# Kernel tuning notes

Measured on AMD Instinct MI355X. Metric: run time of the kernel, lower is better.

The kernel has to match this reference:

```python
import jax, jax.numpy as jnp
import numpy as np

B, S, D, H = 2, 2048, 1024, 16
DK = D // H  # 64
SCALE = DK ** (-0.5)  # NOTE: module divides by this, i.e. multiplies scores by sqrt(DK)


def setup_inputs() -> dict:
    key = jax.random.key(0)
    ks = jax.random.split(key, 9)
    std = D ** (-0.5)
    return {
        "x": jax.random.normal(ks[0], (B, S, D), dtype=jnp.float32),
        "attention_mask": jnp.ones((B, S), dtype=jnp.int32),
        "Wq": jax.random.normal(ks[1], (D, D), dtype=jnp.float32) * std,
        "bq": jnp.zeros((D,), dtype=jnp.float32),
        "Wk": jax.random.normal(ks[2], (D, D), dtype=jnp.float32) * std,
        "bk": jnp.zeros((D,), dtype=jnp.float32),
        "Wv": jax.random.normal(ks[3], (D, D), dtype=jnp.float32) * std,
        "bv": jnp.zeros((D,), dtype=jnp.float32),
        "Wo": jax.random.normal(ks[4], (D, D), dtype=jnp.float32) * std,
        "bo": jnp.zeros((D,), dtype=jnp.float32),
    }


def _split_heads(t):
    # [B, S, D] -> [B, H, S, DK]
    return t.reshape(B, S, H, DK).transpose(0, 2, 1, 3)


def reference(x, attention_mask, Wq, bq, Wk, bk, Wv, bv, Wo, bo):
    q = _split_heads(x @ Wq.T + bq)
    k = _split_heads(x @ Wk.T + bk)
    v = _split_heads(x @ Wv.T + bv)

    # faithful to source: sim = (q @ k^T) / scale with scale = dk**-0.5
    sim = jnp.einsum("bhqd,bhkd->bhqk", q, k) / SCALE

    # key-padding mask: positions where attention_mask == 0 are masked out
    neg = jnp.finfo(sim.dtype).min
    keep = attention_mask.astype(bool)[:, None, None, :]  # [B,1,1,S]
    sim = jnp.where(keep, sim, neg)

    attn = jax.nn.softmax(sim, axis=-1)  # dropout is identity at inference
    out = jnp.einsum("bhqk,bhkd->bhqd", attn, v)
    out = out.transpose(0, 2, 1, 3).reshape(B, S, D)  # merge heads
    return out @ Wo.T + bo
```

## Files before the change

### kernel.cpp

```cpp
#include <hip/hip_runtime.h>
#include <hip/hip_bf16.h>
#include <math.h>

#define BB 2
#define SS 2048
#define DD 1024
#define HH 16
#define DKK 64
#define BH (BB * HH)

typedef __bf16 bf16_t;
typedef _Float16 f16_t;
typedef __attribute__((ext_vector_type(8))) _Float16 f16x8;
typedef __attribute__((ext_vector_type(4))) _Float16 f16x4;
typedef __attribute__((ext_vector_type(4))) float f32x4;
typedef __attribute__((ext_vector_type(4))) int i32x4;
typedef __attribute__((ext_vector_type(2))) int i32x2;

#define GLD_LDS(gp, lp) __builtin_amdgcn_global_load_lds( \
    (const __attribute__((address_space(1))) void*)(gp),  \
    (__attribute__((address_space(3))) void*)(lp), 16, 0, 0)

static __device__ __forceinline__ int pkrtz(float a, float b) {
    auto h = __builtin_amdgcn_cvt_pkrtz(a, b);
    return __builtin_bit_cast(int, h);
}

__global__ void prep_all(const float* __restrict__ x, const int* __restrict__ mask,
                         const float* __restrict__ Wq, const float* __restrict__ Wk,
                         const float* __restrict__ Wv, const float* __restrict__ Wo,
                         f16_t* __restrict__ xf,
                         f16_t* __restrict__ wqkh, f16_t* __restrict__ wqkl,
                         f16_t* __restrict__ wvf, f16_t* __restrict__ wof,
                         int* __restrict__ flags) {
    const int NXi = BB * SS * DD;
    const int NWi = DD * DD;
    const int total = NXi + 4 * NWi;
    int i = blockIdx.x * blockDim.x + threadIdx.x;
    const int stride = gridDim.x * blockDim.x;
    for (; i < total; i += stride) {
        if (i < NXi) {
            xf[i] = (f16_t)x[i];
        } else if (i < NXi + 2 * NWi) {
            const int j = i - NXi;
            const float v = (j < NWi) ? Wq[j] : Wk[j - NWi];
            const f16_t h = (f16_t)v;
            wqkh[j] = h;
            wqkl[j] = (f16_t)(v - (float)h);
        } else {
            const int j = i - NXi - 2 * NWi;
            if (j < NWi) wvf[j] = (f16_t)Wv[j];
            else         wof[j - NWi] = (f16_t)Wo[j - NWi];
        }
    }
    if (blockIdx.x == 0 && threadIdx.x < BB * (SS / 128)) {
        const int f = threadIdx.x;
        const int b = f / (SS / 128), t = f % (SS / 128);
        const int* p = mask + b * SS + t * 128;
        int all = 1;
        for (int j = 0; j < 128; ++j) all &= (p[j] != 0);
        flags[f] = all;
    }
}

__global__ __launch_bounds__(256) void gemm_qkv(const f16_t* __restrict__ Af,
                                                const f16_t* __restrict__ Wqkh,
                                                const f16_t* __restrict__ Wqkl,
                                                const f16_t* __restrict__ Wvf,
                                                const float* __restrict__ bq,
                                                const float* __restrict__ bk,
                                                const float* __restrict__ bv,
                                                f16_t* __restrict__ q_o,
                                                f16_t* __restrict__ k_o,
                                                f16_t* __restrict__ vt_o,
                                                int K) {
    __shared__ __align__(16) f16_t sA[8192];
    __shared__ __align__(16) f16_t sB0[8192];
    __shared__ __align__(16) f16_t sB1[8192];

    const int tid  = threadIdx.x;
    const int wv   = tid >> 6;
    const int lane = tid & 63;
    const int quad = lane >> 4;
    const int l15  = lane & 15;
    const int wr   = wv >> 1;
    const int wc   = wv & 1;
    const int row0 = blockIdx.y * 128;
    const int col0 = blockIdx.x * 128;
    const bool isV = (col0 >= 2048);

    const f16_t* B0 = isV ? (Wvf + (long)(col0 - 2048) * K) : (Wqkh + (long)col0 * K);
    const f16_t* B1 = isV ? nullptr : (Wqkl + (long)col0 * K);

    f32x4 acc[4][4] = {};

    const int srow8 = lane >> 3;
    const int gsw   = ((lane & 7) ^ srow8) * 8;
    const long aoff = (long)(row0 + wv * 8 + srow8) * K + gsw;
    const long boff = (long)(wv * 8 + srow8) * K + gsw;
    const int lsw   = l15 & 7;

    if (isV) {
#pragma unroll 1
        for (int kb = 0; kb < K; kb += 64) {
#pragma unroll
            for (int p = 0; p < 4; ++p) {
                const long go = (long)p * 32 * K + kb;
                const int lo = p * 2048 + wv * 512;
                GLD_LDS(Af + aoff + go, sA + lo);
                GLD_LDS(B0 + boff + go, sB0 + lo);
            }
            __syncthreads();
#pragma unroll
            for (int kk = 0; kk < 2; ++kk) {
                f16x8 af[4];
#pragma unroll
                for (int mt = 0; mt < 4; ++mt)
                    af[mt] = *(const f16x8*)&sA[(wr * 64 + mt * 16 + l15) * 64 + (((kk * 4 + quad) ^ lsw) << 3)];
#pragma unroll
                for (int nt = 0; nt < 4; ++nt) {
                    f16x8 b0 = *(const f16x8*)&sB0[(wc * 64 + nt * 16 + l15) * 64 + (((kk * 4 + quad) ^ lsw) << 3)];
#pragma unroll
                    for (int mt = 0; mt < 4; ++mt)
                        acc[mt][nt] = __builtin_amdgcn_mfma_f32_16x16x32_f16(af[mt], b0, acc[mt][nt], 0, 0, 0);
                }
            }
            __syncthreads();
        }
    } else {
#pragma unroll 1
        for (int kb = 0; kb < K; kb += 64) {
#pragma unroll
            for (int p = 0; p < 4; ++p) {
                const long go = (long)p * 32 * K + kb;
                const int lo = p * 2048 + wv * 512;
                GLD_LDS(Af + aoff + go, sA + lo);
                GLD_LDS(B0 + boff + go, sB0 + lo);
                GLD_LDS(B1 + boff + go, sB1 + lo);
            }
            __syncthreads();
#pragma unroll
            for (int kk = 0; kk < 2; ++kk) {
                f16x8 af[4];
#pragma unroll
                for (int mt = 0; mt < 4; ++mt)
                    af[mt] = *(const f16x8*)&sA[(wr * 64 + mt * 16 + l15) * 64 + (((kk * 4 + quad) ^ lsw) << 3)];
#pragma unroll
                for (int nt = 0; nt < 4; ++nt) {
                    f16x8 b0 = *(const f16x8*)&sB0[(wc * 64 + nt * 16 + l15) * 64 + (((kk * 4 + quad) ^ lsw) << 3)];
                    f16x8 b1 = *(const f16x8*)&sB1[(wc * 64 + nt * 16 + l15) * 64 + (((kk * 4 + quad) ^ lsw) << 3)];
#pragma unroll
                    for (int mt = 0; mt < 4; ++mt) {
                        acc[mt][nt] = __builtin_amdgcn_mfma_f32_16x16x32_f16(af[mt], b0, acc[mt][nt], 0, 0, 0);
                        acc[mt][nt] = __builtin_amdgcn_mfma_f32_16x16x32_f16(af[mt], b1, acc[mt][nt], 0, 0, 0);
                    }
                }
            }
            __syncthreads();
        }
    }

    if (isV) {
#pragma unroll
        for (int nt = 0; nt < 4; ++nt) {
            const int colv = (col0 - 2048) + wc * 64 + nt * 16 + l15;
            const float bvv = bv[colv];
            const int hq = colv >> 6, dk = colv & 63;
#pragma unroll
            for (int mt = 0; mt < 4; ++mt) {
                const int grow0 = row0 + wr * 64 + mt * 16 + quad * 4;
                const int bq2 = grow0 >> 11;
                const int s0  = grow0 & (SS - 1);
                f16x4 pk;
#pragma unroll
                for (int r = 0; r < 4; ++r) pk[r] = (f16_t)(acc[mt][nt][r] + bvv);
                *(f16x4*)(vt_o + ((long)(bq2 * HH + hq) * DKK + dk) * SS + s0) = pk;
            }
        }
    } else {
        const bool isK = (col0 >= 1024);
        const float* bias = isK ? bk : bq;
        f16_t* op = isK ? k_o : q_o;
#pragma unroll
        for (int nt = 0; nt < 4; ++nt) {
            const int gcol = (col0 & 1023) + wc * 64 + nt * 16 + l15;
            const float bvv = bias[gcol];
            const int hq = gcol >> 6, dk = gcol & 63;
#pragma unroll
            for (int mt = 0; mt < 4; ++mt) {
                const int grow0 = row0 + wr * 64 + mt * 16 + quad * 4;
#pragma unroll
                for (int r = 0; r < 4; ++r) {
                    int grow = grow0 + r;
                    float vvv = acc[mt][nt][r] + bvv;
                    long off = (((long)(grow >> 11) * HH + hq) * SS + (grow & (SS - 1))) * DKK + dk;
                    op[off] = (f16_t)vvv;
                }
            }
        }
    }
}

__global__ __launch_bounds__(256) void gemm_o(const f16_t* __restrict__ Ah,
                                              const f16_t* __restrict__ Bhp,
                                              const float* __restrict__ bias,
                                              float* __restrict__ outf,
                                              int N, int K) {
    __shared__ __align__(16) f16_t lds[2048 + 4096];
    f16_t* Ash = lds;
    f16_t* Bsh = lds + 2048;

    const int tid  = threadIdx.x;
    const int wv   = tid >> 6;
    const int lane = tid & 63;
    const int quad = lane >> 4;
    const int l15  = lane & 15;
    const int wr   = wv >> 1;
    const int wc   = wv & 1;
    const int row0 = blockIdx.y * 64;
    const int col0 = blockIdx.x * 128;

    f32x4 acc[2][4] = {};

    const int srow = lane >> 2;
    const int scol = (lane & 3) * 8;
    const f16_t* gA  = Ah  + (long)(row0 + wv * 16 + srow) * K + scol;
    const f16_t* gB0 = Bhp + (long)(col0 + wv * 16 + srow) * K + scol;
    const f16_t* gB1 = Bhp + (long)(col0 + (wv + 4) * 16 + srow) * K + scol;
    f16_t* lA  = Ash + wv * 512;
    f16_t* lB0 = Bsh + wv * 512;
    f16_t* lB1 = Bsh + (wv + 4) * 512;

#pragma unroll 1
    for (int kb = 0; kb < K; kb += 32) {
        GLD_LDS(gA + kb, lA);
        GLD_LDS(gB0 + kb, lB0);
        GLD_LDS(gB1 + kb, lB1);
        __syncthreads();

        f16x8 af[2];
#pragma unroll
        for (int mt = 0; mt < 2; ++mt)
            af[mt] = *(const f16x8*)&Ash[(wr * 32 + mt * 16 + l15) * 32 + quad * 8];
#pragma unroll
        for (int nt = 0; nt < 4; ++nt) {
            f16x8 bh = *(const f16x8*)&Bsh[(wc * 64 + nt * 16 + l15) * 32 + quad * 8];
#pragma unroll
            for (int mt = 0; mt < 2; ++mt)
                acc[mt][nt] = __builtin_amdgcn_mfma_f32_16x16x32_f16(af[mt], bh, acc[mt][nt], 0, 0, 0);
        }
        __syncthreads();
    }

#pragma unroll
    for (int mt = 0; mt < 2; ++mt) {
#pragma unroll
        for (int nt = 0; nt < 4; ++nt) {
            const int gcol  = col0 + wc * 64 + nt * 16 + l15;
            const float bvv = bias[gcol];
            const int grow0 = row0 + wr * 32 + mt * 16 + quad * 4;
#pragma unroll
            for (int r = 0; r < 4; ++r)
                outf[(long)(grow0 + r) * N + gcol] = acc[mt][nt][r] + bvv;
        }
    }
}

__global__ __launch_bounds__(512, 4) void attn_mfma12(const f16_t* __restrict__ Qp,
                                                      const f16_t* __restrict__ Kp,
                                                      const f16_t* __restrict__ Vtp,
                                                      const int* __restrict__ mask,
                                                      const int* __restrict__ flags,
                                                      f16_t* __restrict__ ctx,
                                                      int seq_len) {
    __shared__ __align__(16) f16_t Ksh[2][4096];
    __shared__ __align__(16) f16_t Vsh[2][2][4096];

    const int tid  = threadIdx.x;
    const int wv   = tid >> 6;
    const int lane = tid & 63;
    const int quad = lane >> 4;
    const int l15  = lane & 15;
    const int bh   = blockIdx.y;
    const int b    = bh >> 4;
    const int h    = bh & 15;
    const int q0   = blockIdx.x * 128 + wv * 16;

    const long kb = (long)bh * SS * DKK;

    f16x8 qf[2];
    {
        const f16_t* pq = Qp + kb + (long)(q0 + l15) * DKK + quad * 8;
        qf[0] = *(const f16x8*)pq;
        qf[1] = *(const f16x8*)(pq + 32);
        const f16_t qs = (f16_t)(8.0f * 1.44269504088896f);
#pragma unroll
        for (int j = 0; j < 8; ++j) { qf[0][j] *= qs; qf[1][j] *= qs; }
    }

    f16x4 ones4;
#pragma unroll
    for (int j = 0; j < 4; ++j) ones4[j] = (f16_t)1.0f;

    f32x4 o[4], lacc;
#pragma unroll
    for (int r = 0; r < 4; ++r) o[r] = (f32x4){0.f, 0.f, 0.f, 0.f};
    lacc = (f32x4){0.f, 0.f, 0.f, 0.f};
    float m = -1e30f;

    const int* mrow = mask + b * SS;
    const int* frow = flags + b * (SS / 128);

    const int srow8 = lane >> 3;
    const int gcolB = ((lane & 7) ^ srow8) * 8;
    const int NT = seq_len >> 7;

#pragma unroll
    for (int c = 0; c < 2; ++c) {
        const int row = wv * 8 + srow8;
        GLD_LDS(Kp + kb + (long)(c * 64 + row) * DKK + gcolB, &Ksh[c][wv * 512]);
        GLD_LDS(Vtp + kb + (long)row * SS + c * 64 + gcolB, &Vsh[0][c][wv * 512]);
    }

#pragma unroll 1
    for (int tt = 0; tt < NT; ++tt) {
        const int cur = tt & 1;
        const int kt = tt << 7;
        __syncthreads();

        f32x4 s[8];
#pragma unroll
        for (int nt = 0; nt < 8; ++nt) s[nt] = (f32x4){0.f, 0.f, 0.f, 0.f};
#pragma unroll
        for (int nt = 0; nt < 8; ++nt) {
            const int c = nt >> 2;
            const int kr = (nt & 3) * 16 + l15;
#pragma unroll
            for (int dt = 0; dt < 2; ++dt) {
                f16x8 kf = *(const f16x8*)&Ksh[c][kr * 64 + (((dt * 4 + quad) ^ (l15 & 7)) << 3)];
                s[nt] = __builtin_amdgcn_mfma_f32_16x16x32_f16(kf, qf[dt], s[nt], 0, 0, 0);
            }
        }

        __syncthreads();
        if (tt + 1 < NT) {
            const int kn = (tt + 1) << 7;
#pragma unroll
            for (int c = 0; c < 2; ++c) {
                const int row = wv * 8 + srow8;
                GLD_LDS(Kp + kb + (long)(kn + c * 64 + row) * DKK + gcolB, &Ksh[c][wv * 512]);
                GLD_LDS(Vtp + kb + (long)row * SS + kn + c * 64 + gcolB, &Vsh[cur ^ 1][c][wv * 512]);
            }
        }

        if (!frow[kt >> 7]) {
#pragma unroll
            for (int nt = 0; nt < 8; ++nt) {
                i32x4 kp = *(const i32x4*)&mrow[kt + nt * 16 + quad * 4];
#pragma unroll
                for (int r = 0; r < 4; ++r)
                    s[nt][r] = kp[r] ? s[nt][r] : -1e30f;
            }
        }

        f32x4 mx;
#pragma unroll
        for (int r = 0; r < 4; ++r)
            mx[r] = fmaxf(fmaxf(fmaxf(s[0][r], s[1][r]), fmaxf(s[2][r], s[3][r])),
                          fmaxf(fmaxf(s[4][r], s[5][r]), fmaxf(s[6][r], s[7][r])));
        float tm = fmaxf(fmaxf(mx[0], mx[1]), fmaxf(mx[2], mx[3]));
        tm = fmaxf(tm, __shfl_xor(tm, 16));
        tm = fmaxf(tm, __shfl_xor(tm, 32));

        const float mn = fmaxf(m, tm);
        if (__any(tm > m)) {
            const float alpha = exp2f(m - mn);
            float a4[4];
#pragma unroll
            for (int r = 0; r < 4; ++r) a4[r] = __shfl(alpha, quad * 4 + r);
#pragma unroll
            for (int t = 0; t < 4; ++t)
#pragma unroll
                for (int r = 0; r < 4; ++r) o[t][r] *= a4[r];
#pragma unroll
            for (int r = 0; r < 4; ++r) lacc[r] *= a4[r];
        }
        m = mn;

#pragma unroll
        for (int nt = 0; nt < 8; ++nt) {
            const int c = nt >> 2;
            i32x2 pp;
            pp[0] = pkrtz(exp2f(s[nt][0] - mn), exp2f(s[nt][1] - mn));
            pp[1] = pkrtz(exp2f(s[nt][2] - mn), exp2f(s[nt][3] - mn));
            f16x4 paf = __builtin_bit_cast(f16x4, pp);
            lacc = __builtin_amdgcn_mfma_f32_16x16x16f16(paf, ones4, lacc, 0, 0, 0);
            const int vcol = ((((nt & 3) * 2 + (quad >> 1)) ^ (l15 & 7)) << 3) + ((quad & 1) << 2);
#pragma unroll
            for (int t = 0; t < 4; ++t) {
                f16x4 vB = *(const f16x4*)&Vsh[cur][c][(t * 16 + l15) * 64 + vcol];
                o[t] = __builtin_amdgcn_mfma_f32_16x16x16f16(paf, vB, o[t], 0, 0, 0);
            }
        }
    }

    float inv[4];
#pragma unroll
    for (int r = 0; r < 4; ++r) inv[r] = 1.0f / lacc[r];
#pragma unroll
    for (int t = 0; t < 4; ++t) {
        int d = t * 16 + l15;
#pragma unroll
        for (int r = 0; r < 4; ++r) {
            int tok = b * SS + q0 + quad * 4 + r;
            ctx[(long)tok * DD + h * DKK + d] = (f16_t)(o[t][r] * inv[r]);
        }
    }
}

extern "C" void kernel_launch(void* const* d_in, const int* in_sizes, int n_in,
                              void* d_out, int out_size, void* d_ws, size_t ws_size,
                              hipStream_t stream) {
    const float* x  = (const float*)d_in[0];
    const int* mask = (const int*)d_in[1];
    const float* Wq = (const float*)d_in[2];
    const float* bq = (const float*)d_in[3];
    const float* Wk = (const float*)d_in[4];
    const float* bk = (const float*)d_in[5];
    const float* Wv = (const float*)d_in[6];
    const float* bv = (const float*)d_in[7];
    const float* Wo = (const float*)d_in[8];
    const float* bo = (const float*)d_in[9];
    float* out = (float*)d_out;

    const long NX = (long)BB * SS * DD;
    const long NW = (long)DD * DD;

    char* ws = (char*)d_ws;
    f16_t* xf   = (f16_t*)ws; ws += NX * 2;
    f16_t* wqkh = (f16_t*)ws; ws += 2 * NW * 2;
    f16_t* wqkl = (f16_t*)ws; ws += 2 * NW * 2;
    f16_t* wvf  = (f16_t*)ws; ws += NW * 2;
    f16_t* wof  = (f16_t*)ws; ws += NW * 2;
    f16_t* qf   = (f16_t*)ws; ws += NX * 2;
    f16_t* kf   = (f16_t*)ws; ws += NX * 2;
    f16_t* vt   = (f16_t*)ws; ws += NX * 2;
    f16_t* ctx  = (f16_t*)ws; ws += NX * 2;
    int*   flg  = (int*)ws;   ws += 64 * 4;

    prep_all<<<2048, 256, 0, stream>>>(x, mask, Wq, Wk, Wv, Wo,
                                       xf, wqkh, wqkl, wvf, wof, flg);

    dim3 gqkv(3 * DD / 128, (BB * SS) / 128);
    gemm_qkv<<<gqkv, 256, 0, stream>>>(xf, wqkh, wqkl, wvf, bq, bk, bv, qf, kf, vt, DD);

    dim3 agrid(SS / 128, BH);
    attn_mfma12<<<agrid, 512, 0, stream>>>(qf, kf, vt, mask, flg, ctx, SS);

    dim3 go(DD / 128, (BB * SS) / 64);
    gemm_o<<<go, 256, 0, stream>>>(ctx, wof, bo, out, DD, DD);
}
```

Baseline: 249.2 us.

## Double K-tile depth with XOR-swizzled LDS in output GEMM; lazy softmax rescale

The output-projection GEMM now loads a 64-wide K slice per iteration instead of 32. It stores A and B tiles in LDS with an XOR swizzle to avoid bank conflicts, which halves the number of barriers per K sweep. Separately, the attention kernel skips rescaling of the running output and denominator unless the new row max exceeds the old one by more than 8 in log2 space. That lazy-rescale threshold relies on fp16 probabilities tolerating values up to 2^8 before overflow risk, which trades some numerical headroom for fewer rescale passes.

```diff
diff --git a/kernel.cpp b/kernel.cpp
--- a/kernel.cpp
+++ b/kernel.cpp
@@ -206,9 +206,8 @@
                                               const float* __restrict__ bias,
                                               float* __restrict__ outf,
                                               int N, int K) {
-    __shared__ __align__(16) f16_t lds[2048 + 4096];
-    f16_t* Ash = lds;
-    f16_t* Bsh = lds + 2048;
+    __shared__ __align__(16) f16_t sA[4096];
+    __shared__ __align__(16) f16_t sB[8192];
 
     const int tid  = threadIdx.x;
     const int wv   = tid >> 6;
@@ -222,32 +221,37 @@
 
     f32x4 acc[2][4] = {};
 
-    const int srow = lane >> 2;
-    const int scol = (lane & 3) * 8;
-    const f16_t* gA  = Ah  + (long)(row0 + wv * 16 + srow) * K + scol;
-    const f16_t* gB0 = Bhp + (long)(col0 + wv * 16 + srow) * K + scol;
-    const f16_t* gB1 = Bhp + (long)(col0 + (wv + 4) * 16 + srow) * K + scol;
-    f16_t* lA  = Ash + wv * 512;
-    f16_t* lB0 = Bsh + wv * 512;
-    f16_t* lB1 = Bsh + (wv + 4) * 512;
+    const int srow8 = lane >> 3;
+    const int gsw   = ((lane & 7) ^ srow8) * 8;
+    const long aoff = (long)(row0 + wv * 8 + srow8) * K + gsw;
+    const long boff = (long)(col0 + wv * 8 + srow8) * K + gsw;
+    const int lsw   = l15 & 7;
 
 #pragma unroll 1
-    for (int kb = 0; kb < K; kb += 32) {
-        GLD_LDS(gA + kb, lA);
-        GLD_LDS(gB0 + kb, lB0);
-        GLD_LDS(gB1 + kb, lB1);
+    for (int kb = 0; kb < K; kb += 64) {
+#pragma unroll
+        for (int p = 0; p < 2; ++p) {
+            GLD_LDS(Ah + aoff + (long)p * 32 * K + kb, sA + p * 2048 + wv * 512);
+        }
+#pragma unroll
+        for (int p = 0; p < 4; ++p) {
+            GLD_LDS(Bhp + boff + (long)p * 32 * K + kb, sB + p * 2048 + wv * 512);
+        }
         __syncthreads();
 
-        f16x8 af[2];
-#pragma unroll
-        for (int mt = 0; mt < 2; ++mt)
-            af[mt] = *(const f16x8*)&Ash[(wr * 32 + mt * 16 + l15) * 32 + quad * 8];
-#pragma unroll
-        for (int nt = 0; nt < 4; ++nt) {
-            f16x8 bh = *(const f16x8*)&Bsh[(wc * 64 + nt * 16 + l15) * 32 + quad * 8];
+#pragma unroll
+        for (int kk = 0; kk < 2; ++kk) {
+            f16x8 af[2];
 #pragma unroll
             for (int mt = 0; mt < 2; ++mt)
-                acc[mt][nt] = __builtin_amdgcn_mfma_f32_16x16x32_f16(af[mt], bh, acc[mt][nt], 0, 0, 0);
+                af[mt] = *(const f16x8*)&sA[(wr * 32 + mt * 16 + l15) * 64 + (((kk * 4 + quad) ^ lsw) << 3)];
+#pragma unroll
+            for (int nt = 0; nt < 4; ++nt) {
+                f16x8 bh = *(const f16x8*)&sB[(wc * 64 + nt * 16 + l15) * 64 + (((kk * 4 + quad) ^ lsw) << 3)];
+#pragma unroll
+                for (int mt = 0; mt < 2; ++mt)
+                    acc[mt][nt] = __builtin_amdgcn_mfma_f32_16x16x32_f16(af[mt], bh, acc[mt][nt], 0, 0, 0);
+            }
         }
         __syncthreads();
     }
@@ -266,7 +270,7 @@
     }
 }
 
-__global__ __launch_bounds__(512, 4) void attn_mfma12(const f16_t* __restrict__ Qp,
+__global__ __launch_bounds__(512, 4) void attn_mfma13(const f16_t* __restrict__ Qp,
                                                       const f16_t* __restrict__ Kp,
                                                       const f16_t* __restrict__ Vtp,
                                                       const int* __restrict__ mask,
@@ -372,8 +376,8 @@
         tm = fmaxf(tm, __shfl_xor(tm, 16));
         tm = fmaxf(tm, __shfl_xor(tm, 32));
 
-        const float mn = fmaxf(m, tm);
-        if (__any(tm > m)) {
+        if (__any(tm > m + 8.0f)) {
+            const float mn = fmaxf(m, tm);
             const float alpha = exp2f(m - mn);
             float a4[4];
 #pragma unroll
@@ -384,15 +388,15 @@
                 for (int r = 0; r < 4; ++r) o[t][r] *= a4[r];
 #pragma unroll
             for (int r = 0; r < 4; ++r) lacc[r] *= a4[r];
-        }
-        m = mn;
+            m = mn;
+        }
 
 #pragma unroll
         for (int nt = 0; nt < 8; ++nt) {
             const int c = nt >> 2;
             i32x2 pp;
-            pp[0] = pkrtz(exp2f(s[nt][0] - mn), exp2f(s[nt][1] - mn));
-            pp[1] = pkrtz(exp2f(s[nt][2] - mn), exp2f(s[nt][3] - mn));
+            pp[0] = pkrtz(exp2f(s[nt][0] - m), exp2f(s[nt][1] - m));
+            pp[1] = pkrtz(exp2f(s[nt][2] - m), exp2f(s[nt][3] - m));
             f16x4 paf = __builtin_bit_cast(f16x4, pp);
             lacc = __builtin_amdgcn_mfma_f32_16x16x16f16(paf, ones4, lacc, 0, 0, 0);
             const int vcol = ((((nt & 3) * 2 + (quad >> 1)) ^ (l15 & 7)) << 3) + ((quad & 1) << 2);
@@ -455,7 +459,7 @@
     gemm_qkv<<<gqkv, 256, 0, stream>>>(xf, wqkh, wqkl, wvf, bq, bk, bv, qf, kf, vt, DD);
 
     dim3 agrid(SS / 128, BH);
-    attn_mfma12<<<agrid, 512, 0, stream>>>(qf, kf, vt, mask, flg, ctx, SS);
+    attn_mfma13<<<agrid, 512, 0, stream>>>(qf, kf, vt, mask, flg, ctx, SS);
 
     dim3 go(DD / 128, (BB * SS) / 64);
     gemm_o<<<go, 256, 0, stream>>>(ctx, wof, bo, out, DD, DD);
```

New measurement: 239.6 us. -3.8%, faster.
